# Optimization experiments

Measured on AMD Instinct MI355X. Metric: run time of the kernel, lower is better.

## Reference

```python
import jax, jax.numpy as jnp
import numpy as np

N = 50000
E = 800000
NFEAT, NHID, NCLASS = 128, 64, 16


def _spmm(row, col, w, x):
    # out[i] = sum_{e: row[e]==i} w[e] * x[col[e]]  -- sparse adj @ x
    return jax.ops.segment_sum(x[col] * w[:, None], row, num_segments=N)


def _gcn_layer(x, row, col, w, W, b):
    return _spmm(row, col, w, x @ W) + b


def setup_inputs() -> dict:
    key = jax.random.key(0)
    ks = jax.random.split(key, 16)
    glorot = lambda k, fi, fo: jax.random.uniform(k, (fi, fo), jnp.float32, -1.0, 1.0) / jnp.sqrt(fi)
    inp = {
        "x": jax.random.normal(ks[0], (N, NFEAT), jnp.float32),
        "edge_row": jax.random.randint(ks[1], (E,), 0, N, jnp.int32),
        "edge_col": jax.random.randint(ks[2], (E,), 0, N, jnp.int32),
        "edge_weight": jax.random.uniform(ks[3], (E,), jnp.float32),
        "W1": glorot(ks[4], NFEAT, NHID), "b1": jnp.zeros((NHID,), jnp.float32),
        "W2": glorot(ks[5], NHID, NHID), "b2": jnp.zeros((NHID,), jnp.float32),
        "W3": glorot(ks[6], NHID, NHID), "b3": jnp.zeros((NHID,), jnp.float32),
        "W4": glorot(ks[7], NHID, NHID), "b4": jnp.zeros((NHID,), jnp.float32),
        "W5": glorot(ks[8], NHID, NCLASS), "b5": jnp.zeros((NCLASS,), jnp.float32),
    }
    return inp


def reference(x, edge_row, edge_col, edge_weight, W1, b1, W2, b2, W3, b3, W4, b4, W5, b5):
    # Inference mode: dropout is identity.
    e1 = _gcn_layer(x, edge_row, edge_col, edge_weight, W1, b1)
    h = jax.nn.relu(e1)
    e2 = _gcn_layer(h, edge_row, edge_col, edge_weight, W2, b2)
    h = jax.nn.relu(e2)
    e3 = _gcn_layer(h, edge_row, edge_col, edge_weight, W3, b3)
    h = jax.nn.relu(e3)
    e4 = _gcn_layer(h, edge_row, edge_col, edge_weight, W4, b4)
    h = jax.nn.relu(e4)
    e5 = _gcn_layer(h, edge_row, edge_col, edge_weight, W5, b5)
    return (jax.nn.log_softmax(e5, axis=1), e1, e2, e3, e4, e5)
```

## Files before the change

### kernel.cpp

```cpp
#include <hip/hip_runtime.h>
#include <math.h>

#define NN 50000
#define NE 800000
#define NFEAT 128
#define NHID 64
#define NCLASS 16
#define NB_SCAN ((NN + 255) / 256)
#define ROWS_PER_GRP 6250
#define GB ((NN + 63) / 64)
#define SCHUNKS 392

struct alignas(8) Edge {
    int c;
    float w;
};

__device__ inline unsigned short f2bf(float f) {
    unsigned u = __builtin_bit_cast(unsigned, f);
    u += 0x7fffu + ((u >> 16) & 1u);
    return (unsigned short)(u >> 16);
}
__device__ inline float bf2f(unsigned short h) {
    return __builtin_bit_cast(float, (unsigned)h << 16);
}


__global__ __launch_bounds__(256) void hist_rank_kernel(const int* __restrict__ erow,
                                                        int* __restrict__ deg,
                                                        unsigned* __restrict__ rr, int E) {
    int e = blockIdx.x * 256 + threadIdx.x;
    if (e < E) {
        int r = erow[e];
        int k = atomicAdd(&deg[r], 1);
        rr[e] = ((unsigned)r << 16) | (unsigned)k;
    }
}

__global__ __launch_bounds__(256) void scan_sum_kernel(const int* __restrict__ deg,
                                                       int* __restrict__ blocksum, int n) {
    __shared__ int s[256];
    const int t = threadIdx.x;
    int i = blockIdx.x * 256 + t;
    s[t] = (i < n) ? deg[i] : 0;
    __syncthreads();
#pragma unroll
    for (int off = 128; off > 0; off >>= 1) {
        if (t < off) s[t] += s[t + off];
        __syncthreads();
    }
    if (t == 0) blocksum[blockIdx.x] = s[0];
}

__global__ __launch_bounds__(256) void scan_top_kernel(int* __restrict__ blocksum, int nb) {
    __shared__ int s[256];
    const int t = threadIdx.x;
    int v = (t < nb) ? blocksum[t] : 0;
    s[t] = v;
    __syncthreads();
    for (int off = 1; off < 256; off <<= 1) {
        int u = (t >= off) ? s[t - off] : 0;
        __syncthreads();
        s[t] += u;
        __syncthreads();
    }
    if (t < nb) blocksum[t] = s[t] - v;
}

__global__ __launch_bounds__(256) void scan_final_kernel(const int* __restrict__ deg,
                                                         const int* __restrict__ blocksum,
                                                         int* __restrict__ row_ptr, int n) {
    __shared__ int s[256];
    const int t = threadIdx.x;
    int i = blockIdx.x * 256 + t;
    int d = (i < n) ? deg[i] : 0;
    s[t] = d;
    __syncthreads();
    for (int off = 1; off < 256; off <<= 1) {
        int u = (t >= off) ? s[t - off] : 0;
        __syncthreads();
        s[t] += u;
        __syncthreads();
    }
    int excl = blocksum[blockIdx.x] + s[t] - d;
    if (i < n) {
        row_ptr[i] = excl;
        if (i == n - 1) row_ptr[n] = excl + d;
    }
}

__global__ __launch_bounds__(256) void scatter_rank_kernel(const unsigned* __restrict__ rr,
                                                           const int* __restrict__ ecol,
                                                           const float* __restrict__ ew,
                                                           const int* __restrict__ row_ptr,
                                                           Edge* __restrict__ pairs, int E) {
    const int g = blockIdx.x & 7;
    const int chunk = blockIdx.x >> 3;
    const int CH = (E + SCHUNKS - 1) / SCHUNKS;
    const int lo = chunk * CH;
    const int hi = (lo + CH < E) ? lo + CH : E;
    for (int e = lo + threadIdx.x; e < hi; e += 256) {
        unsigned v = rr[e];
        int r = (int)(v >> 16);
        if (r / ROWS_PER_GRP == g) {
            int pos = row_ptr[r] + (int)(v & 0xffffu);
            Edge p;
            p.c = ecol[e];
            p.w = ew[e];
            pairs[pos] = p;
        }
    }
}

template <int K, bool RELU_IN>
__global__ __launch_bounds__(256) void gemm64_kernel(const float* __restrict__ in,
                                                     const float* __restrict__ Wg,
                                                     unsigned short* __restrict__ outb, int M) {
    constexpr int KC = 64;
    __shared__ float xs[KC][68];
    __shared__ float Ws[KC][64];
    const int t = threadIdx.x;
    const int tx = t % 16;
    const int ty = t / 16;
    const int r0 = blockIdx.x * 64;

    float acc[4][4];
#pragma unroll
    for (int i = 0; i < 4; i++)
#pragma unroll
        for (int j = 0; j < 4; j++) acc[i][j] = 0.f;

    for (int k0 = 0; k0 < K; k0 += KC) {
        for (int i = t * 4; i < KC * 64; i += 1024) {
            *(float4*)&Ws[i / 64][i % 64] = *(const float4*)&Wg[(size_t)k0 * 64 + i];
        }
        {
            const int r = t / 4;
            const int q = t % 4;
            const int gr = r0 + r;
#pragma unroll
            for (int i = 0; i < 4; i++) {
                int k = q * 16 + i * 4;
                float4 v;
                if (gr < M)
                    v = *(const float4*)&in[(size_t)gr * K + k0 + k];
                else
                    v = make_float4(0.f, 0.f, 0.f, 0.f);
                if (RELU_IN) {
                    v.x = fmaxf(v.x, 0.f);
                    v.y = fmaxf(v.y, 0.f);
                    v.z = fmaxf(v.z, 0.f);
                    v.w = fmaxf(v.w, 0.f);
                }
                xs[k + 0][r] = v.x;
                xs[k + 1][r] = v.y;
                xs[k + 2][r] = v.z;
                xs[k + 3][r] = v.w;
            }
        }
        __syncthreads();
#pragma unroll 8
        for (int k = 0; k < KC; k++) {
            float4 xv = *(const float4*)&xs[k][ty * 4];
            float4 wv = *(const float4*)&Ws[k][tx * 4];
            acc[0][0] += xv.x * wv.x; acc[0][1] += xv.x * wv.y;
            acc[0][2] += xv.x * wv.z; acc[0][3] += xv.x * wv.w;
            acc[1][0] += xv.y * wv.x; acc[1][1] += xv.y * wv.y;
            acc[1][2] += xv.y * wv.z; acc[1][3] += xv.y * wv.w;
            acc[2][0] += xv.z * wv.x; acc[2][1] += xv.z * wv.y;
            acc[2][2] += xv.z * wv.z; acc[2][3] += xv.z * wv.w;
            acc[3][0] += xv.w * wv.x; acc[3][1] += xv.w * wv.y;
            acc[3][2] += xv.w * wv.z; acc[3][3] += xv.w * wv.w;
        }
        __syncthreads();
    }
#pragma unroll
    for (int i = 0; i < 4; i++) {
        int r = r0 + ty * 4 + i;
        if (r < M) {
            ushort4 u;
            u.x = f2bf(acc[i][0]);
            u.y = f2bf(acc[i][1]);
            u.z = f2bf(acc[i][2]);
            u.w = f2bf(acc[i][3]);
            *(ushort4*)&outb[(size_t)r * 64 + tx * 4] = u;
        }
    }
}

template <int K, int NOUT, int RPT, bool RELU_IN>
__global__ __launch_bounds__(256) void gemm_kernel(const float* __restrict__ in,
                                                   const float* __restrict__ Wg,
                                                   float* __restrict__ out, int M) {
    __shared__ float Wl[K * NOUT];
    for (int i = threadIdx.x * 4; i < K * NOUT; i += 256 * 4) {
        *(float4*)&Wl[i] = *(const float4*)&Wg[i];
    }
    __syncthreads();

    constexpr int GROUPS = 256 / NOUT;
    constexpr int RPB = GROUPS * RPT;
    const int col = threadIdx.x % NOUT;
    const int grp = threadIdx.x / NOUT;
    const int r = blockIdx.x * RPB + grp * RPT;
    if (r >= M) return;

    float acc[RPT];
#pragma unroll
    for (int j = 0; j < RPT; j++) acc[j] = 0.f;

    const float* pr = in + (size_t)r * K;
#pragma unroll 2
    for (int k = 0; k < K; k += 4) {
        float w0 = Wl[(k + 0) * NOUT + col];
        float w1 = Wl[(k + 1) * NOUT + col];
        float w2 = Wl[(k + 2) * NOUT + col];
        float w3 = Wl[(k + 3) * NOUT + col];
#pragma unroll
        for (int j = 0; j < RPT; j++) {
            float4 xv = *(const float4*)(pr + j * K + k);
            if (RELU_IN) {
                xv.x = fmaxf(xv.x, 0.f);
                xv.y = fmaxf(xv.y, 0.f);
                xv.z = fmaxf(xv.z, 0.f);
                xv.w = fmaxf(xv.w, 0.f);
            }
            acc[j] += xv.x * w0;
            acc[j] += xv.y * w1;
            acc[j] += xv.z * w2;
            acc[j] += xv.w * w3;
        }
    }
#pragma unroll
    for (int j = 0; j < RPT; j++) {
        if (r + j < M) out[(size_t)(r + j) * NOUT + col] = acc[j];
    }
}

__global__ __launch_bounds__(256) void spmm64v2_kernel(const unsigned short* __restrict__ tmpb,
                                                       const int* __restrict__ row_ptr,
                                                       const Edge* __restrict__ pairs,
                                                       const float* __restrict__ bias,
                                                       float* __restrict__ e_out, int M) {
    const int t = threadIdx.x;
    const int r = blockIdx.x * 8 + (t >> 5);
    if (r >= M) return;
    const int f2 = (t & 31) * 2;

    int e = row_ptr[r];
    const int end = row_ptr[r + 1];
    float a0 = 0.f, a1 = 0.f;
    for (; e + 7 < end; e += 8) {
        Edge p0 = pairs[e + 0], p1 = pairs[e + 1], p2 = pairs[e + 2], p3 = pairs[e + 3];
        Edge p4 = pairs[e + 4], p5 = pairs[e + 5], p6 = pairs[e + 6], p7 = pairs[e + 7];
        unsigned g0 = *(const unsigned*)&tmpb[(size_t)p0.c * 64 + f2];
        unsigned g1 = *(const unsigned*)&tmpb[(size_t)p1.c * 64 + f2];
        unsigned g2 = *(const unsigned*)&tmpb[(size_t)p2.c * 64 + f2];
        unsigned g3 = *(const unsigned*)&tmpb[(size_t)p3.c * 64 + f2];
        unsigned g4 = *(const unsigned*)&tmpb[(size_t)p4.c * 64 + f2];
        unsigned g5 = *(const unsigned*)&tmpb[(size_t)p5.c * 64 + f2];
        unsigned g6 = *(const unsigned*)&tmpb[(size_t)p6.c * 64 + f2];
        unsigned g7 = *(const unsigned*)&tmpb[(size_t)p7.c * 64 + f2];
        a0 += p0.w * bf2f((unsigned short)(g0 & 0xffffu));
        a1 += p0.w * bf2f((unsigned short)(g0 >> 16));
        a0 += p1.w * bf2f((unsigned short)(g1 & 0xffffu));
        a1 += p1.w * bf2f((unsigned short)(g1 >> 16));
        a0 += p2.w * bf2f((unsigned short)(g2 & 0xffffu));
        a1 += p2.w * bf2f((unsigned short)(g2 >> 16));
        a0 += p3.w * bf2f((unsigned short)(g3 & 0xffffu));
        a1 += p3.w * bf2f((unsigned short)(g3 >> 16));
        a0 += p4.w * bf2f((unsigned short)(g4 & 0xffffu));
        a1 += p4.w * bf2f((unsigned short)(g4 >> 16));
        a0 += p5.w * bf2f((unsigned short)(g5 & 0xffffu));
        a1 += p5.w * bf2f((unsigned short)(g5 >> 16));
        a0 += p6.w * bf2f((unsigned short)(g6 & 0xffffu));
        a1 += p6.w * bf2f((unsigned short)(g6 >> 16));
        a0 += p7.w * bf2f((unsigned short)(g7 & 0xffffu));
        a1 += p7.w * bf2f((unsigned short)(g7 >> 16));
    }
    for (; e < end; e++) {
        Edge p = pairs[e];
        unsigned g = *(const unsigned*)&tmpb[(size_t)p.c * 64 + f2];
        a0 += p.w * bf2f((unsigned short)(g & 0xffffu));
        a1 += p.w * bf2f((unsigned short)(g >> 16));
    }
    float2 v;
    v.x = a0 + bias[f2];
    v.y = a1 + bias[f2 + 1];
    *(float2*)&e_out[(size_t)r * 64 + f2] = v;
}

__global__ __launch_bounds__(256) void spmm16_lsm_kernel(const float* __restrict__ tmp,
                                                         const int* __restrict__ row_ptr,
                                                         const Edge* __restrict__ pairs,
                                                         const float* __restrict__ bias,
                                                         float* __restrict__ e5,
                                                         float* __restrict__ out0, int M) {
    const int f = threadIdx.x & 15;
    const int rl = threadIdx.x >> 4;
    const int r = blockIdx.x * 16 + rl;
    if (r >= M) return;

    const int start = row_ptr[r];
    const int end = row_ptr[r + 1];
    float acc = 0.f;
    int e = start;
    for (; e + 3 < end; e += 4) {
        Edge p0 = pairs[e + 0], p1 = pairs[e + 1], p2 = pairs[e + 2], p3 = pairs[e + 3];
        acc += p0.w * tmp[(size_t)p0.c * 16 + f];
        acc += p1.w * tmp[(size_t)p1.c * 16 + f];
        acc += p2.w * tmp[(size_t)p2.c * 16 + f];
        acc += p3.w * tmp[(size_t)p3.c * 16 + f];
    }
    for (; e < end; e++) {
        Edge p = pairs[e];
        acc += p.w * tmp[(size_t)p.c * 16 + f];
    }
    float v = acc + bias[f];
    e5[(size_t)r * 16 + f] = v;

    float m = v;
#pragma unroll
    for (int off = 1; off < 16; off <<= 1) m = fmaxf(m, __shfl_xor(m, off, 16));
    float s = expf(v - m);
#pragma unroll
    for (int off = 1; off < 16; off <<= 1) s += __shfl_xor(s, off, 16);
    float ls = logf(s);
    out0[(size_t)r * 16 + f] = v - m - ls;
}


extern "C" void kernel_launch(void* const* d_in, const int* in_sizes, int n_in,
                              void* d_out, int out_size, void* d_ws, size_t ws_size,
                              hipStream_t stream) {
    const float* x = (const float*)d_in[0];
    const int* erow = (const int*)d_in[1];
    const int* ecol = (const int*)d_in[2];
    const float* ew = (const float*)d_in[3];
    const float* W1 = (const float*)d_in[4];
    const float* b1 = (const float*)d_in[5];
    const float* W2 = (const float*)d_in[6];
    const float* b2 = (const float*)d_in[7];
    const float* W3 = (const float*)d_in[8];
    const float* b3 = (const float*)d_in[9];
    const float* W4 = (const float*)d_in[10];
    const float* b4 = (const float*)d_in[11];
    const float* W5 = (const float*)d_in[12];
    const float* b5 = (const float*)d_in[13];

    float* out0 = (float*)d_out;
    float* e1 = out0 + (size_t)NN * NCLASS;
    float* e2 = e1 + (size_t)NN * NHID;
    float* e3 = e2 + (size_t)NN * NHID;
    float* e4 = e3 + (size_t)NN * NHID;
    float* e5 = e4 + (size_t)NN * NHID;

    char* ws = (char*)d_ws;
    unsigned short* tmpb = (unsigned short*)ws; ws += (size_t)NN * NHID * 2;
    float* tmp32 = (float*)ws; ws += (size_t)NN * NCLASS * sizeof(float);
    int* deg = (int*)ws;       ws += ((size_t)NN * 4 + 255) / 256 * 256;
    int* row_ptr = (int*)ws;   ws += ((size_t)(NN + 1) * 4 + 255) / 256 * 256;
    int* blocksum = (int*)ws;  ws += ((size_t)NB_SCAN * 4 + 255) / 256 * 256;
    unsigned* rr = (unsigned*)ws; ws += (size_t)NE * 4;
    Edge* pairs = (Edge*)ws;   ws += (size_t)NE * sizeof(Edge);

    hipMemsetAsync(deg, 0, (size_t)NN * 4, stream);
    hist_rank_kernel<<<(NE + 255) / 256, 256, 0, stream>>>(erow, deg, rr, NE);
    scan_sum_kernel<<<NB_SCAN, 256, 0, stream>>>(deg, blocksum, NN);
    scan_top_kernel<<<1, 256, 0, stream>>>(blocksum, NB_SCAN);
    scan_final_kernel<<<NB_SCAN, 256, 0, stream>>>(deg, blocksum, row_ptr, NN);
    scatter_rank_kernel<<<8 * SCHUNKS, 256, 0, stream>>>(rr, ecol, ew, row_ptr, pairs, NE);

    gemm64_kernel<NFEAT, false><<<GB, 256, 0, stream>>>(x, W1, tmpb, NN);
    spmm64v2_kernel<<<(NN + 7) / 8, 256, 0, stream>>>(tmpb, row_ptr, pairs, b1, e1, NN);

    gemm64_kernel<NHID, true><<<GB, 256, 0, stream>>>(e1, W2, tmpb, NN);
    spmm64v2_kernel<<<(NN + 7) / 8, 256, 0, stream>>>(tmpb, row_ptr, pairs, b2, e2, NN);

    gemm64_kernel<NHID, true><<<GB, 256, 0, stream>>>(e2, W3, tmpb, NN);
    spmm64v2_kernel<<<(NN + 7) / 8, 256, 0, stream>>>(tmpb, row_ptr, pairs, b3, e3, NN);

    gemm64_kernel<NHID, true><<<GB, 256, 0, stream>>>(e3, W4, tmpb, NN);
    spmm64v2_kernel<<<(NN + 7) / 8, 256, 0, stream>>>(tmpb, row_ptr, pairs, b4, e4, NN);

    gemm_kernel<NHID, NCLASS, 4, true><<<GB, 256, 0, stream>>>(e4, W5, tmp32, NN);
    spmm16_lsm_kernel<<<(NN + 15) / 16, 256, 0, stream>>>(tmp32, row_ptr, pairs, b5, e5, out0, NN);
}
```

Before: 360.8 us.

## Pack edge column and bf16 weight into 32 bits, fuse scan top pass

Edge records shrink from an 8-byte int/float pair to a 32-bit word holding a 16-bit column index and a bf16 weight. This halves edge-list traffic in every sparse aggregation pass. The top-level scan is folded into the final scan kernel to drop a launch, and the scatter uses four row groups instead of eight. The last layer's dense output is stored as bf16 and its sparse loop is unrolled by eight. Rounding edge weights to bf16 adds numerical error, and the 16-bit column relies on the node count staying below 65536.

```diff
diff --git a/kernel.cpp b/kernel.cpp
--- a/kernel.cpp
+++ b/kernel.cpp
@@ -7,14 +7,10 @@
 #define NHID 64
 #define NCLASS 16
 #define NB_SCAN ((NN + 255) / 256)
-#define ROWS_PER_GRP 6250
 #define GB ((NN + 63) / 64)
+#define SGRP 4
+#define ROWS_PER_SGRP ((NN + SGRP - 1) / SGRP)
 #define SCHUNKS 392
-
-struct alignas(8) Edge {
-    int c;
-    float w;
-};
 
 __device__ inline unsigned short f2bf(float f) {
     unsigned u = __builtin_bit_cast(unsigned, f);
@@ -24,6 +20,8 @@
 __device__ inline float bf2f(unsigned short h) {
     return __builtin_bit_cast(float, (unsigned)h << 16);
 }
+__device__ inline float pk_w(unsigned v) { return bf2f((unsigned short)(v >> 16)); }
+__device__ inline int pk_c(unsigned v) { return (int)(v & 0xffffu); }
 
 
 __global__ __launch_bounds__(256) void hist_rank_kernel(const int* __restrict__ erow,
@@ -52,26 +50,22 @@
     if (t == 0) blocksum[blockIdx.x] = s[0];
 }
 
-__global__ __launch_bounds__(256) void scan_top_kernel(int* __restrict__ blocksum, int nb) {
-    __shared__ int s[256];
-    const int t = threadIdx.x;
-    int v = (t < nb) ? blocksum[t] : 0;
-    s[t] = v;
-    __syncthreads();
-    for (int off = 1; off < 256; off <<= 1) {
-        int u = (t >= off) ? s[t - off] : 0;
-        __syncthreads();
-        s[t] += u;
-        __syncthreads();
-    }
-    if (t < nb) blocksum[t] = s[t] - v;
-}
-
 __global__ __launch_bounds__(256) void scan_final_kernel(const int* __restrict__ deg,
                                                          const int* __restrict__ blocksum,
                                                          int* __restrict__ row_ptr, int n) {
+    __shared__ int bs[256];
     __shared__ int s[256];
     const int t = threadIdx.x;
+    bs[t] = (t < NB_SCAN) ? blocksum[t] : 0;
+    __syncthreads();
+    for (int off = 1; off < 256; off <<= 1) {
+        int u = (t >= off) ? bs[t - off] : 0;
+        __syncthreads();
+        bs[t] += u;
+        __syncthreads();
+    }
+    const int blockpre = (blockIdx.x == 0) ? 0 : bs[blockIdx.x - 1];
+
     int i = blockIdx.x * 256 + t;
     int d = (i < n) ? deg[i] : 0;
     s[t] = d;
@@ -82,7 +76,7 @@
         s[t] += u;
         __syncthreads();
     }
-    int excl = blocksum[blockIdx.x] + s[t] - d;
+    int excl = blockpre + s[t] - d;
     if (i < n) {
         row_ptr[i] = excl;
         if (i == n - 1) row_ptr[n] = excl + d;
@@ -93,21 +87,18 @@
                                                            const int* __restrict__ ecol,
                                                            const float* __restrict__ ew,
                                                            const int* __restrict__ row_ptr,
-                                                           Edge* __restrict__ pairs, int E) {
-    const int g = blockIdx.x & 7;
-    const int chunk = blockIdx.x >> 3;
+                                                           unsigned* __restrict__ pk, int E) {
+    const int g = blockIdx.x & (SGRP - 1);
+    const int chunk = blockIdx.x / SGRP;
     const int CH = (E + SCHUNKS - 1) / SCHUNKS;
     const int lo = chunk * CH;
     const int hi = (lo + CH < E) ? lo + CH : E;
     for (int e = lo + threadIdx.x; e < hi; e += 256) {
         unsigned v = rr[e];
         int r = (int)(v >> 16);
-        if (r / ROWS_PER_GRP == g) {
+        if (r / ROWS_PER_SGRP == g) {
             int pos = row_ptr[r] + (int)(v & 0xffffu);
-            Edge p;
-            p.c = ecol[e];
-            p.w = ew[e];
-            pairs[pos] = p;
+            pk[pos] = ((unsigned)f2bf(ew[e]) << 16) | (unsigned)ecol[e];
         }
     }
 }
@@ -189,9 +180,9 @@
 }
 
 template <int K, int NOUT, int RPT, bool RELU_IN>
-__global__ __launch_bounds__(256) void gemm_kernel(const float* __restrict__ in,
-                                                   const float* __restrict__ Wg,
-                                                   float* __restrict__ out, int M) {
+__global__ __launch_bounds__(256) void gemm16_kernel(const float* __restrict__ in,
+                                                     const float* __restrict__ Wg,
+                                                     unsigned short* __restrict__ outb, int M) {
     __shared__ float Wl[K * NOUT];
     for (int i = threadIdx.x * 4; i < K * NOUT; i += 256 * 4) {
         *(float4*)&Wl[i] = *(const float4*)&Wg[i];
@@ -233,13 +224,13 @@
     }
 #pragma unroll
     for (int j = 0; j < RPT; j++) {
-        if (r + j < M) out[(size_t)(r + j) * NOUT + col] = acc[j];
+        if (r + j < M) outb[(size_t)(r + j) * NOUT + col] = f2bf(acc[j]);
     }
 }
 
 __global__ __launch_bounds__(256) void spmm64v2_kernel(const unsigned short* __restrict__ tmpb,
                                                        const int* __restrict__ row_ptr,
-                                                       const Edge* __restrict__ pairs,
+                                                       const unsigned* __restrict__ pk,
                                                        const float* __restrict__ bias,
                                                        float* __restrict__ e_out, int M) {
     const int t = threadIdx.x;
@@ -251,38 +242,38 @@
     const int end = row_ptr[r + 1];
     float a0 = 0.f, a1 = 0.f;
     for (; e + 7 < end; e += 8) {
-        Edge p0 = pairs[e + 0], p1 = pairs[e + 1], p2 = pairs[e + 2], p3 = pairs[e + 3];
-        Edge p4 = pairs[e + 4], p5 = pairs[e + 5], p6 = pairs[e + 6], p7 = pairs[e + 7];
-        unsigned g0 = *(const unsigned*)&tmpb[(size_t)p0.c * 64 + f2];
-        unsigned g1 = *(const unsigned*)&tmpb[(size_t)p1.c * 64 + f2];
-        unsigned g2 = *(const unsigned*)&tmpb[(size_t)p2.c * 64 + f2];
-        unsigned g3 = *(const unsigned*)&tmpb[(size_t)p3.c * 64 + f2];
-        unsigned g4 = *(const unsigned*)&tmpb[(size_t)p4.c * 64 + f2];
-        unsigned g5 = *(const unsigned*)&tmpb[(size_t)p5.c * 64 + f2];
-        unsigned g6 = *(const unsigned*)&tmpb[(size_t)p6.c * 64 + f2];
-        unsigned g7 = *(const unsigned*)&tmpb[(size_t)p7.c * 64 + f2];
-        a0 += p0.w * bf2f((unsigned short)(g0 & 0xffffu));
-        a1 += p0.w * bf2f((unsigned short)(g0 >> 16));
-        a0 += p1.w * bf2f((unsigned short)(g1 & 0xffffu));
-        a1 += p1.w * bf2f((unsigned short)(g1 >> 16));
-        a0 += p2.w * bf2f((unsigned short)(g2 & 0xffffu));
-        a1 += p2.w * bf2f((unsigned short)(g2 >> 16));
-        a0 += p3.w * bf2f((unsigned short)(g3 & 0xffffu));
-        a1 += p3.w * bf2f((unsigned short)(g3 >> 16));
-        a0 += p4.w * bf2f((unsigned short)(g4 & 0xffffu));
-        a1 += p4.w * bf2f((unsigned short)(g4 >> 16));
-        a0 += p5.w * bf2f((unsigned short)(g5 & 0xffffu));
-        a1 += p5.w * bf2f((unsigned short)(g5 >> 16));
-        a0 += p6.w * bf2f((unsigned short)(g6 & 0xffffu));
-        a1 += p6.w * bf2f((unsigned short)(g6 >> 16));
-        a0 += p7.w * bf2f((unsigned short)(g7 & 0xffffu));
-        a1 += p7.w * bf2f((unsigned short)(g7 >> 16));
+        unsigned q0 = pk[e + 0], q1 = pk[e + 1], q2 = pk[e + 2], q3 = pk[e + 3];
+        unsigned q4 = pk[e + 4], q5 = pk[e + 5], q6 = pk[e + 6], q7 = pk[e + 7];
+        unsigned g0 = *(const unsigned*)&tmpb[(size_t)pk_c(q0) * 64 + f2];
+        unsigned g1 = *(const unsigned*)&tmpb[(size_t)pk_c(q1) * 64 + f2];
+        unsigned g2 = *(const unsigned*)&tmpb[(size_t)pk_c(q2) * 64 + f2];
+        unsigned g3 = *(const unsigned*)&tmpb[(size_t)pk_c(q3) * 64 + f2];
+        unsigned g4 = *(const unsigned*)&tmpb[(size_t)pk_c(q4) * 64 + f2];
+        unsigned g5 = *(const unsigned*)&tmpb[(size_t)pk_c(q5) * 64 + f2];
+        unsigned g6 = *(const unsigned*)&tmpb[(size_t)pk_c(q6) * 64 + f2];
+        unsigned g7 = *(const unsigned*)&tmpb[(size_t)pk_c(q7) * 64 + f2];
+        a0 += pk_w(q0) * bf2f((unsigned short)(g0 & 0xffffu));
+        a1 += pk_w(q0) * bf2f((unsigned short)(g0 >> 16));
+        a0 += pk_w(q1) * bf2f((unsigned short)(g1 & 0xffffu));
+        a1 += pk_w(q1) * bf2f((unsigned short)(g1 >> 16));
+        a0 += pk_w(q2) * bf2f((unsigned short)(g2 & 0xffffu));
+        a1 += pk_w(q2) * bf2f((unsigned short)(g2 >> 16));
+        a0 += pk_w(q3) * bf2f((unsigned short)(g3 & 0xffffu));
+        a1 += pk_w(q3) * bf2f((unsigned short)(g3 >> 16));
+        a0 += pk_w(q4) * bf2f((unsigned short)(g4 & 0xffffu));
+        a1 += pk_w(q4) * bf2f((unsigned short)(g4 >> 16));
+        a0 += pk_w(q5) * bf2f((unsigned short)(g5 & 0xffffu));
+        a1 += pk_w(q5) * bf2f((unsigned short)(g5 >> 16));
+        a0 += pk_w(q6) * bf2f((unsigned short)(g6 & 0xffffu));
+        a1 += pk_w(q6) * bf2f((unsigned short)(g6 >> 16));
+        a0 += pk_w(q7) * bf2f((unsigned short)(g7 & 0xffffu));
+        a1 += pk_w(q7) * bf2f((unsigned short)(g7 >> 16));
     }
     for (; e < end; e++) {
-        Edge p = pairs[e];
-        unsigned g = *(const unsigned*)&tmpb[(size_t)p.c * 64 + f2];
-        a0 += p.w * bf2f((unsigned short)(g & 0xffffu));
-        a1 += p.w * bf2f((unsigned short)(g >> 16));
+        unsigned q = pk[e];
+        unsigned g = *(const unsigned*)&tmpb[(size_t)pk_c(q) * 64 + f2];
+        a0 += pk_w(q) * bf2f((unsigned short)(g & 0xffffu));
+        a1 += pk_w(q) * bf2f((unsigned short)(g >> 16));
     }
     float2 v;
     v.x = a0 + bias[f2];
@@ -290,9 +281,9 @@
     *(float2*)&e_out[(size_t)r * 64 + f2] = v;
 }
 
-__global__ __launch_bounds__(256) void spmm16_lsm_kernel(const float* __restrict__ tmp,
+__global__ __launch_bounds__(256) void spmm16_lsm_kernel(const unsigned short* __restrict__ tmpc,
                                                          const int* __restrict__ row_ptr,
-                                                         const Edge* __restrict__ pairs,
+                                                         const unsigned* __restrict__ pk,
                                                          const float* __restrict__ bias,
                                                          float* __restrict__ e5,
                                                          float* __restrict__ out0, int M) {
@@ -301,20 +292,24 @@
     const int r = blockIdx.x * 16 + rl;
     if (r >= M) return;
 
-    const int start = row_ptr[r];
+    int e = row_ptr[r];
     const int end = row_ptr[r + 1];
     float acc = 0.f;
-    int e = start;
-    for (; e + 3 < end; e += 4) {
-        Edge p0 = pairs[e + 0], p1 = pairs[e + 1], p2 = pairs[e + 2], p3 = pairs[e + 3];
-        acc += p0.w * tmp[(size_t)p0.c * 16 + f];
-        acc += p1.w * tmp[(size_t)p1.c * 16 + f];
-        acc += p2.w * tmp[(size_t)p2.c * 16 + f];
-        acc += p3.w * tmp[(size_t)p3.c * 16 + f];
+    for (; e + 7 < end; e += 8) {
+        unsigned q0 = pk[e + 0], q1 = pk[e + 1], q2 = pk[e + 2], q3 = pk[e + 3];
+        unsigned q4 = pk[e + 4], q5 = pk[e + 5], q6 = pk[e + 6], q7 = pk[e + 7];
+        acc += pk_w(q0) * bf2f(tmpc[(size_t)pk_c(q0) * 16 + f]);
+        acc += pk_w(q1) * bf2f(tmpc[(size_t)pk_c(q1) * 16 + f]);
+        acc += pk_w(q2) * bf2f(tmpc[(size_t)pk_c(q2) * 16 + f]);
+        acc += pk_w(q3) * bf2f(tmpc[(size_t)pk_c(q3) * 16 + f]);
+        acc += pk_w(q4) * bf2f(tmpc[(size_t)pk_c(q4) * 16 + f]);
+        acc += pk_w(q5) * bf2f(tmpc[(size_t)pk_c(q5) * 16 + f]);
+        acc += pk_w(q6) * bf2f(tmpc[(size_t)pk_c(q6) * 16 + f]);
+        acc += pk_w(q7) * bf2f(tmpc[(size_t)pk_c(q7) * 16 + f]);
     }
     for (; e < end; e++) {
-        Edge p = pairs[e];
-        acc += p.w * tmp[(size_t)p.c * 16 + f];
+        unsigned q = pk[e];
+        acc += pk_w(q) * bf2f(tmpc[(size_t)pk_c(q) * 16 + f]);
     }
     float v = acc + bias[f];
     e5[(size_t)r * 16 + f] = v;
@@ -357,32 +352,31 @@
 
     char* ws = (char*)d_ws;
     unsigned short* tmpb = (unsigned short*)ws; ws += (size_t)NN * NHID * 2;
-    float* tmp32 = (float*)ws; ws += (size_t)NN * NCLASS * sizeof(float);
+    unsigned short* tmpc = (unsigned short*)ws; ws += ((size_t)NN * NCLASS * 2 + 255) / 256 * 256;
     int* deg = (int*)ws;       ws += ((size_t)NN * 4 + 255) / 256 * 256;
     int* row_ptr = (int*)ws;   ws += ((size_t)(NN + 1) * 4 + 255) / 256 * 256;
     int* blocksum = (int*)ws;  ws += ((size_t)NB_SCAN * 4 + 255) / 256 * 256;
     unsigned* rr = (unsigned*)ws; ws += (size_t)NE * 4;
-    Edge* pairs = (Edge*)ws;   ws += (size_t)NE * sizeof(Edge);
+    unsigned* pk = (unsigned*)ws; ws += (size_t)NE * 4;
 
     hipMemsetAsync(deg, 0, (size_t)NN * 4, stream);
     hist_rank_kernel<<<(NE + 255) / 256, 256, 0, stream>>>(erow, deg, rr, NE);
     scan_sum_kernel<<<NB_SCAN, 256, 0, stream>>>(deg, blocksum, NN);
-    scan_top_kernel<<<1, 256, 0, stream>>>(blocksum, NB_SCAN);
     scan_final_kernel<<<NB_SCAN, 256, 0, stream>>>(deg, blocksum, row_ptr, NN);
-    scatter_rank_kernel<<<8 * SCHUNKS, 256, 0, stream>>>(rr, ecol, ew, row_ptr, pairs, NE);
+    scatter_rank_kernel<<<SGRP * SCHUNKS, 256, 0, stream>>>(rr, ecol, ew, row_ptr, pk, NE);
 
     gemm64_kernel<NFEAT, false><<<GB, 256, 0, stream>>>(x, W1, tmpb, NN);
-    spmm64v2_kernel<<<(NN + 7) / 8, 256, 0, stream>>>(tmpb, row_ptr, pairs, b1, e1, NN);
+    spmm64v2_kernel<<<(NN + 7) / 8, 256, 0, stream>>>(tmpb, row_ptr, pk, b1, e1, NN);
 
     gemm64_kernel<NHID, true><<<GB, 256, 0, stream>>>(e1, W2, tmpb, NN);
-    spmm64v2_kernel<<<(NN + 7) / 8, 256, 0, stream>>>(tmpb, row_ptr, pairs, b2, e2, NN);
+    spmm64v2_kernel<<<(NN + 7) / 8, 256, 0, stream>>>(tmpb, row_ptr, pk, b2, e2, NN);
 
     gemm64_kernel<NHID, true><<<GB, 256, 0, stream>>>(e2, W3, tmpb, NN);
-    spmm64v2_kernel<<<(NN + 7) / 8, 256, 0, stream>>>(tmpb, row_ptr, pairs, b3, e3, NN);
+    spmm64v2_kernel<<<(NN + 7) / 8, 256, 0, stream>>>(tmpb, row_ptr, pk, b3, e3, NN);
 
     gemm64_kernel<NHID, true><<<GB, 256, 0, stream>>>(e3, W4, tmpb, NN);
-    spmm64v2_kernel<<<(NN + 7) / 8, 256, 0, stream>>>(tmpb, row_ptr, pairs, b4, e4, NN);
-
-    gemm_kernel<NHID, NCLASS, 4, true><<<GB, 256, 0, stream>>>(e4, W5, tmp32, NN);
-    spmm16_lsm_kernel<<<(NN + 15) / 16, 256, 0, stream>>>(tmp32, row_ptr, pairs, b5, e5, out0, NN);
-}
+    spmm64v2_kernel<<<(NN + 7) / 8, 256, 0, stream>>>(tmpb, row_ptr, pk, b4, e4, NN);
+
+    gemm16_kernel<NHID, NCLASS, 4, true><<<GB, 256, 0, stream>>>(e4, W5, tmpc, NN);
+    spmm16_lsm_kernel<<<(NN + 15) / 16, 256, 0, stream>>>(tmpc, row_ptr, pk, b5, e5, out0, NN);
+}
```

After: 344.2 us. -4.6%, faster.
